# Kernel tuning notes

Measured on AMD Instinct MI355X. Metric: run time of the kernel, lower is better.

## Reference

```python
import jax, jax.numpy as jnp
import numpy as np

D = 1024   # dims
H = 16     # heads
HD = D // H  # head_dim = 64
F = HD // 2  # rotary frequency count


def _layernorm(x, g, b, eps=1e-5):
    m = x.mean(-1, keepdims=True)
    v = jnp.mean((x - m) ** 2, axis=-1, keepdims=True)
    return (x - m) * jax.lax.rsqrt(v + eps) * g + b


def _freq_base():
    # mask=None branch of rotary._compute_freqs: mel-style frequencies
    mel_max = 2595.0 * np.log10(1.0 + 4000.0 / 200.0)
    scale = 10.0 ** (np.linspace(0.0, mel_max, F) / 2595.0) - 1.0
    return jnp.asarray(200.0 * scale / 1000.0, dtype=jnp.float32)  # [F]


def _rope_polar(xh, radius, theta):
    # xh: [b,h,c,hd]; radius: [b,c] (learned per-token magnitude); theta: [c,F]
    # complex multiply of interleaved pairs by r*exp(i*theta)
    b_, h_, c_, hd_ = xh.shape
    xp = xh.reshape(b_, h_, c_, F, 2)
    xr, xi = xp[..., 0], xp[..., 1]
    cos = jnp.cos(theta)[None, None]  # [1,1,c,F]
    sin = jnp.sin(theta)[None, None]
    r = radius[:, None, :, None]      # [b,1,c,1]
    out_r = r * (xr * cos - xi * sin)
    out_i = r * (xr * sin + xi * cos)
    return jnp.stack([out_r, out_i], axis=-1).reshape(b_, h_, c_, hd_)


def setup_inputs() -> dict:
    key = jax.random.key(0)
    ks = jax.random.split(key, 6)
    B, C = 2, 2048
    s = 0.02
    return {
        "x": jax.random.normal(ks[0], (B, C, D), jnp.float32),
        "ln_q_g": jnp.ones((D,), jnp.float32),
        "ln_q_b": jnp.zeros((D,), jnp.float32),
        "Wq": jax.random.normal(ks[1], (D, D), jnp.float32) * s,
        "bq": jnp.zeros((D,), jnp.float32),
        "ln_kv_g": jnp.ones((D,), jnp.float32),
        "ln_kv_b": jnp.zeros((D,), jnp.float32),
        "Wkv": jax.random.normal(ks[2], (D, 2 * D), jnp.float32) * s,
        "bkv": jnp.zeros((2 * D,), jnp.float32),
        "Wout": jax.random.normal(ks[3], (D, D), jnp.float32) * s,
        "bout": jnp.zeros((D,), jnp.float32),
        "lnh_g": jnp.ones((HD,), jnp.float32),
        "lnh_b": jnp.zeros((HD,), jnp.float32),
        "Wr": jax.random.normal(ks[4], (D, 1), jnp.float32) * s,
        "br": jnp.zeros((1,), jnp.float32),
    }


def reference(x, ln_q_g, ln_q_b, Wq, bq, ln_kv_g, ln_kv_b, Wkv, bkv,
              Wout, bout, lnh_g, lnh_b, Wr, br):
    B, C, _ = x.shape
    # q path: norm -> linear -> [b,h,c,d]
    q = (_layernorm(x, ln_q_g, ln_q_b) @ Wq + bq).reshape(B, C, H, HD).transpose(0, 2, 1, 3)
    # kv path: norm -> linear -> [2,b,h,c,d]
    kv = (_layernorm(x, ln_kv_g, ln_kv_b) @ Wkv + bkv).reshape(B, C, 2, H, HD).transpose(2, 0, 3, 1, 4)
    k, v = kv[0], kv[1]
    # polar RoPE with learned per-token radius (xa = x for both q and k)
    t = jnp.arange(C, dtype=jnp.float32)
    theta = t[:, None] * _freq_base()[None, :]               # [C,F]
    per_step = (x @ Wr + br)[..., 0]                         # [B,C]
    radius = jnp.clip(per_step / 100.0, 0.5, 2.0)
    q = _rope_polar(q, radius, theta)
    k = _rope_polar(k, radius, theta)
    # per-head LayerNorm fused into SDPA inputs
    qn = _layernorm(q, lnh_g, lnh_b)
    kn = _layernorm(k, lnh_g, lnh_b)
    # non-causal SDPA (torch default scale = 1/sqrt(head_dim))
    logits = jnp.einsum('bhqd,bhkd->bhqk', qn, kn) / jnp.sqrt(jnp.float32(HD))
    attn = jax.nn.softmax(logits, axis=-1)
    o = jnp.einsum('bhqk,bhkd->bhqd', attn, v)
    o = o.transpose(0, 2, 1, 3).reshape(B, C, D)
    return o @ Wout + bout
```

## Files before the change

kernel.cpp:

```cpp
#include <hip/hip_runtime.h>
#include <math.h>

#define D_MODEL 1024
#define NHEADS  16
#define HEADD   64
#define NFREQ   32
#define BATCH   2
#define CSEQ    2048
#define NROWS   (BATCH*CSEQ)
#define NQKV    (3*D_MODEL)

typedef _Float16 half8  __attribute__((ext_vector_type(8)));
typedef _Float16 half4v __attribute__((ext_vector_type(4)));
typedef float    f32x4  __attribute__((ext_vector_type(4)));

__device__ __forceinline__ void async16(void* lds, const void* g)
{
    __builtin_amdgcn_global_load_lds((const __attribute__((address_space(1))) unsigned int*)g,
                                     (__attribute__((address_space(3))) unsigned int*)lds,
                                     16, 0, 0);
}

__global__ __launch_bounds__(256) void build_cs_kernel(float2* __restrict__ cs)
{
    int i = blockIdx.x * 256 + threadIdx.x;
    if (i >= CSEQ * NFREQ) return;
    int c = i >> 5, f = i & (NFREQ - 1);
    double mel_max = 2595.0 * log10(21.0);
    double step    = mel_max / (double)(NFREQ - 1);
    double freq    = 200.0 * (pow(10.0, step * (double)f / 2595.0) - 1.0) / 1000.0;
    float fr = (float)freq;
    float th = (float)c * fr;
    float s, co;
    sincosf(th, &s, &co);
    cs[i] = make_float2(co, s);
}

__global__ __launch_bounds__(256) void bias_init_kernel(
    const float* __restrict__ bq, const float* __restrict__ bkv, float* __restrict__ be)
{
    int i = blockIdx.x * 256 + threadIdx.x;
    if (i < D_MODEL) be[i] = bq[i];
    else if (i < NQKV) be[i] = bkv[i - D_MODEL];
}

__global__ __launch_bounds__(256) void transpose_fold_kernel(
    const float* __restrict__ in, _Float16* __restrict__ out, int R, int C,
    int rowoff, const float* __restrict__ scale,
    const float* __restrict__ bfold, float* __restrict__ bias_acc)
{
    __shared__ float t[32][33];
    __shared__ float part[4][32];
    int bx = blockIdx.x * 32;
    int by = blockIdx.y * 32;
    int tx = threadIdx.x, ty = threadIdx.y;
    #pragma unroll
    for (int i = ty; i < 32; i += 8)
        t[i][tx] = in[(size_t)(by + i) * C + bx + tx];
    __syncthreads();
    float sc = scale ? scale[by + tx] : 1.f;
    #pragma unroll
    for (int i = ty; i < 32; i += 8)
        out[(size_t)(rowoff + bx + i) * R + by + tx] = (_Float16)(t[tx][i] * sc);
    if (bfold) {
        float p = 0.f;
        #pragma unroll
        for (int i = ty; i < 32; i += 8)
            p += bfold[by + i] * t[i][tx];
        p += __shfl_xor(p, 32);
        if ((ty & 1) == 0) part[ty >> 1][tx] = p;
        __syncthreads();
        if (ty == 0)
            atomicAdd(&bias_acc[rowoff + bx + tx],
                      part[0][tx] + part[1][tx] + part[2][tx] + part[3][tx]);
    }
}

__global__ __launch_bounds__(256) void ln_radius_kernel(
    const float* __restrict__ x,
    const float* __restrict__ Wr,  const float* __restrict__ br,
    _Float16* __restrict__ xn, float* __restrict__ radius)
{
    int row = blockIdx.x;
    int tid = threadIdx.x;
    float4 xv = ((const float4*)(x + (size_t)row * D_MODEL))[tid];
    float4 wv = ((const float4*)Wr)[tid];
    float s  = xv.x + xv.y + xv.z + xv.w;
    float ss = xv.x*xv.x + xv.y*xv.y + xv.z*xv.z + xv.w*xv.w;
    float dr = xv.x*wv.x + xv.y*wv.y + xv.z*wv.z + xv.w*wv.w;
    #pragma unroll
    for (int off = 1; off < 64; off <<= 1) {
        s  += __shfl_xor(s, off);
        ss += __shfl_xor(ss, off);
        dr += __shfl_xor(dr, off);
    }
    __shared__ float red[3][4];
    int w = tid >> 6, lane = tid & 63;
    if (lane == 0) { red[0][w] = s; red[1][w] = ss; red[2][w] = dr; }
    __syncthreads();
    s  = red[0][0] + red[0][1] + red[0][2] + red[0][3];
    ss = red[1][0] + red[1][1] + red[1][2] + red[1][3];
    float mean = s * (1.f / D_MODEL);
    float var  = ss * (1.f / D_MODEL) - mean * mean;
    float rinv = rsqrtf(var + 1e-5f);
    half4v o4 = { (_Float16)((xv.x - mean) * rinv), (_Float16)((xv.y - mean) * rinv),
                  (_Float16)((xv.z - mean) * rinv), (_Float16)((xv.w - mean) * rinv) };
    *(half4v*)&xn[(size_t)row * D_MODEL + tid * 4] = o4;
    if (tid == 0) {
        float drt = red[2][0] + red[2][1] + red[2][2] + red[2][3];
        float p = (drt + br[0]) * 0.01f;
        radius[row] = fminf(fmaxf(p, 0.5f), 2.0f);
    }
}

__device__ __forceinline__ void gemm_core32(
    const _Float16* __restrict__ A, const _Float16* __restrict__ B,
    int bm, int bn, int K, _Float16* As, _Float16* Bs, f32x4 (*acc)[4])
{
    int tid = threadIdx.x, lane = tid & 63, w = tid >> 6;
    int wm = w >> 1, wn = w & 1;
    int l15 = lane & 15, lg = lane >> 4;
    int sr  = lane >> 2;
    int sch = lane & 3;

    auto stage = [&](int buf, int k0) {
        #pragma unroll
        for (int i = 0; i < 2; ++i) {
            int seg = w * 2 + i;
            int row = seg * 16 + sr;
            async16(&As[buf * 4096 + seg * 512], &A[(size_t)(bm + row) * K + k0 + sch * 8]);
            async16(&Bs[buf * 4096 + seg * 512], &B[(size_t)(bn + row) * K + k0 + sch * 8]);
        }
    };

    stage(0, 0);
    __syncthreads();
    int cur = 0;
    for (int k0 = 0; k0 < K; k0 += 32) {
        if (k0 + 32 < K) stage(cur ^ 1, k0 + 32);
        half8 af[4], bf[4];
        #pragma unroll
        for (int m = 0; m < 4; ++m)
            af[m] = *(const half8*)&As[cur * 4096 + (wm * 64 + m * 16 + l15) * 32 + lg * 8];
        #pragma unroll
        for (int n = 0; n < 4; ++n)
            bf[n] = *(const half8*)&Bs[cur * 4096 + (wn * 64 + n * 16 + l15) * 32 + lg * 8];
        #pragma unroll
        for (int m = 0; m < 4; ++m)
            #pragma unroll
            for (int n = 0; n < 4; ++n)
                acc[m][n] = __builtin_amdgcn_mfma_f32_16x16x32_f16(af[m], bf[n], acc[m][n], 0, 0, 0);
        __syncthreads();
        cur ^= 1;
    }
}

#define QSCALE 0.18033688f

__global__ __launch_bounds__(256, 4) void gemm_qkv_kernel(
    const _Float16* __restrict__ xn,  const _Float16* __restrict__ WT,
    const float* __restrict__ bias_eff,
    const float* __restrict__ radius, const float2* __restrict__ cs_tab,
    const float* __restrict__ lnh_g,  const float* __restrict__ lnh_b,
    _Float16* __restrict__ qn, _Float16* __restrict__ kn, _Float16* __restrict__ v_rm)
{
    __shared__ _Float16 As[2 * 4096];
    __shared__ _Float16 Bs[2 * 4096];
    int orig = blockIdx.x;
    int wg = (orig & 7) * 96 + (orig >> 3);
    int bm = (wg / 24) * 128;
    int bn = (wg % 24) * 128;

    f32x4 acc[4][4];
    f32x4 z = {0.f, 0.f, 0.f, 0.f};
    #pragma unroll
    for (int m = 0; m < 4; ++m)
        #pragma unroll
        for (int n = 0; n < 4; ++n) acc[m][n] = z;

    gemm_core32(xn, WT, bm, bn, D_MODEL, As, Bs, acc);

    int tid = threadIdx.x, lane = tid & 63, w = tid >> 6;
    int wm = w >> 1, wn = w & 1;
    int l15 = lane & 15, lg = lane >> 4;
    int colbase = bn + wn * 64;

    float bb4[4];
    #pragma unroll
    for (int n = 0; n < 4; ++n) bb4[n] = bias_eff[colbase + n * 16 + l15];

    if (colbase >= 2 * D_MODEL) {
        int vcolb = colbase - 2 * D_MODEL;
        #pragma unroll
        for (int m = 0; m < 4; ++m)
            #pragma unroll
            for (int r = 0; r < 4; ++r) {
                int row = bm + wm * 64 + m * 16 + lg * 4 + r;
                #pragma unroll
                for (int n = 0; n < 4; ++n)
                    v_rm[(size_t)row * D_MODEL + vcolb + n * 16 + l15] =
                        (_Float16)(acc[m][n][r] + bb4[n]);
            }
        return;
    }

    bool isq = colbase < D_MODEL;
    int h = (colbase & (D_MODEL - 1)) >> 6;
    _Float16* dst = isq ? qn : kn;
    float qs = isq ? QSCALE : 1.f;
    bool im = (l15 & 1) != 0;

    float g4[4], bh4[4];
    #pragma unroll
    for (int n = 0; n < 4; ++n) {
        g4[n]  = lnh_g[n * 16 + l15];
        bh4[n] = lnh_b[n * 16 + l15];
    }

    #pragma unroll
    for (int m = 0; m < 4; ++m)
        #pragma unroll
        for (int r = 0; r < 4; ++r) {
            int row = bm + wm * 64 + m * 16 + lg * 4 + r;
            int b = row >> 11, c = row & (CSEQ - 1);
            float rr = radius[row];
            float vals[4];
            float s = 0.f, ss = 0.f;
            #pragma unroll
            for (int n = 0; n < 4; ++n) {
                float v0 = acc[m][n][r] + bb4[n];
                float pr = __shfl_xor(v0, 1);
                float2 cs = cs_tab[c * NFREQ + ((n * 16 + l15) >> 1)];
                float xr_ = im ? pr : v0;
                float xi_ = im ? v0 : pr;
                float rot = im ? rr * (xr_ * cs.y + xi_ * cs.x)
                               : rr * (xr_ * cs.x - xi_ * cs.y);
                vals[n] = rot;
                s += rot; ss += rot * rot;
            }
            #pragma unroll
            for (int off = 1; off < 16; off <<= 1) {
                s  += __shfl_xor(s, off);
                ss += __shfl_xor(ss, off);
            }
            float mean = s * (1.f / 64.f);
            float var  = ss * (1.f / 64.f) - mean * mean;
            float ri   = rsqrtf(var + 1e-5f);
            size_t base = ((size_t)(b * NHEADS + h) * CSEQ + c) * HEADD;
            #pragma unroll
            for (int n = 0; n < 4; ++n) {
                float o = ((vals[n] - mean) * ri * g4[n] + bh4[n]) * qs;
                dst[base + n * 16 + l15] = (_Float16)o;
            }
        }
}

__global__ __launch_bounds__(256, 4) void gemm_out_kernel(
    const _Float16* __restrict__ A, const _Float16* __restrict__ BT,
    const float* __restrict__ bias, float* __restrict__ C)
{
    __shared__ _Float16 As[2 * 4096];
    __shared__ _Float16 Bs[2 * 4096];
    int orig = blockIdx.x;
    int wg = (orig & 7) * 32 + (orig >> 3);
    int bm = (wg >> 3) * 128;
    int bn = (wg & 7) * 128;

    f32x4 acc[4][4];
    f32x4 z = {0.f, 0.f, 0.f, 0.f};
    #pragma unroll
    for (int m = 0; m < 4; ++m)
        #pragma unroll
        for (int n = 0; n < 4; ++n) acc[m][n] = z;

    gemm_core32(A, BT, bm, bn, D_MODEL, As, Bs, acc);

    int tid = threadIdx.x, lane = tid & 63, w = tid >> 6;
    int wm = w >> 1, wn = w & 1;
    int l15 = lane & 15, lg = lane >> 4;
    #pragma unroll
    for (int m = 0; m < 4; ++m) {
        int row = bm + wm * 64 + m * 16 + lg * 4;
        #pragma unroll
        for (int n = 0; n < 4; ++n) {
            int col = bn + wn * 64 + n * 16 + l15;
            float bb = bias[col];
            #pragma unroll
            for (int r = 0; r < 4; ++r)
                C[(size_t)(row + r) * D_MODEL + col] = acc[m][n][r] + bb;
        }
    }
}

__global__ __launch_bounds__(256) void v_transpose_f16(
    const _Float16* __restrict__ v_rm, _Float16* __restrict__ vT)
{
    int bh = blockIdx.x >> 5;
    int c0 = (blockIdx.x & 31) * 64;
    int b = bh >> 4, h = bh & 15;
    __shared__ _Float16 t[64][68];
    int tid = threadIdx.x;
    int dcol = tid & 63, quarter = tid >> 6;
    for (int c = quarter; c < 64; c += 4)
        t[c][dcol] = v_rm[(size_t)(b * CSEQ + c0 + c) * D_MODEL + h * HEADD + dcol];
    __syncthreads();
    for (int d = quarter; d < 64; d += 4)
        vT[(size_t)(bh * HEADD + d) * CSEQ + c0 + dcol] = t[dcol][d];
}

#define KVB 64
#define NT  (CSEQ / KVB)
#define C8L2E 11.541560f

__global__ __launch_bounds__(256, 4) void attn_kernel(
    const _Float16* __restrict__ qn, const _Float16* __restrict__ kn,
    const _Float16* __restrict__ vT, _Float16* __restrict__ o)
{
    __shared__ _Float16 KsB[2][KVB * 64];
    __shared__ _Float16 VsB[2][KVB * 64];
    __shared__ _Float16 P[4][16 * 64];
    int tid = threadIdx.x, lane = tid & 63, w = tid >> 6;
    int l15 = lane & 15, lg = lane >> 4;

    int orig = blockIdx.x;
    int wg   = (orig & 7) * 128 + (orig >> 3);
    int bh   = wg >> 5;
    int qc   = wg & 31;
    int q0   = qc * 64 + w * 16;

    const _Float16* qh = qn + (size_t)bh * CSEQ * HEADD;
    const _Float16* kh = kn + (size_t)bh * CSEQ * HEADD;
    const _Float16* vh = vT + (size_t)bh * HEADD * CSEQ;

    half8 aq[2];
    #pragma unroll
    for (int ks = 0; ks < 2; ++ks)
        aq[ks] = *(const half8*)&qh[(size_t)(q0 + l15) * HEADD + ks * 32 + lg * 8];

    f32x4 z = {0.f, 0.f, 0.f, 0.f};
    f32x4 oacc[4];
    #pragma unroll
    for (int d4 = 0; d4 < 4; ++d4) oacc[d4] = z;
    float lrun = 0.f;

    int srow_in = lane >> 3;
    int csrc    = (lane & 7) ^ srow_in;
    int lsw     = l15 & 7;

    auto stage = [&](int buf, int kt) {
        int k0 = kt * KVB;
        #pragma unroll
        for (int i = 0; i < 2; ++i) {
            int seg = w * 2 + i;
            int r = seg * 8 + srow_in;
            async16(&KsB[buf][seg * 512], &kh[(size_t)(k0 + r) * HEADD + csrc * 8]);
            async16(&VsB[buf][seg * 512], &vh[(size_t)r * CSEQ + k0 + csrc * 8]);
        }
    };

    stage(0, 0);
    __syncthreads();
    int cur = 0;

    for (int kt = 0; kt < NT; ++kt) {
        if (kt + 1 < NT) stage(cur ^ 1, kt + 1);

        f32x4 st[4];
        #pragma unroll
        for (int n = 0; n < 4; ++n) st[n] = f32x4{-C8L2E, -C8L2E, -C8L2E, -C8L2E};
        #pragma unroll
        for (int ks = 0; ks < 2; ++ks) {
            half8 ak[4];
            #pragma unroll
            for (int n = 0; n < 4; ++n) {
                int row = n * 16 + l15;
                int ch = (ks * 4 + lg) ^ (row & 7);
                ak[n] = *(const half8*)&KsB[cur][row * 64 + ch * 8];
            }
            #pragma unroll
            for (int n = 0; n < 4; ++n)
                st[n] = __builtin_amdgcn_mfma_f32_16x16x32_f16(ak[n], aq[ks], st[n], 0, 0, 0);
        }

        float ps = 0.f;
        #pragma unroll
        for (int n = 0; n < 4; ++n)
            #pragma unroll
            for (int r = 0; r < 4; ++r) {
                float e = exp2f(st[n][r]);
                st[n][r] = e;
                ps += e;
            }
        ps += __shfl_xor(ps, 16);
        ps += __shfl_xor(ps, 32);
        lrun += ps;

        #pragma unroll
        for (int n = 0; n < 4; ++n) {
            half4v pk;
            #pragma unroll
            for (int r = 0; r < 4; ++r) pk[r] = (_Float16)st[n][r];
            int t  = n * 2 + (lg >> 1);
            int tp = t ^ lsw;
            *(half4v*)&P[w][l15 * 64 + tp * 8 + (lg & 1) * 4] = pk;
        }

        #pragma unroll
        for (int ks = 0; ks < 2; ++ks) {
            int tp2 = (ks * 4 + lg) ^ lsw;
            half8 ap = *(const half8*)&P[w][l15 * 64 + tp2 * 8];
            half8 bv[4];
            #pragma unroll
            for (int d4 = 0; d4 < 4; ++d4) {
                int row = d4 * 16 + l15;
                int ch = (ks * 4 + lg) ^ (row & 7);
                bv[d4] = *(const half8*)&VsB[cur][row * 64 + ch * 8];
            }
            #pragma unroll
            for (int d4 = 0; d4 < 4; ++d4)
                oacc[d4] = __builtin_amdgcn_mfma_f32_16x16x32_f16(ap, bv[d4], oacc[d4], 0, 0, 0);
        }

        __syncthreads();
        cur ^= 1;
    }

    int b = bh >> 4, h = bh & 15;
    #pragma unroll
    for (int r = 0; r < 4; ++r) {
        float lr = __shfl(lrun, lg * 4 + r);
        float inv = 1.f / lr;
        int c = q0 + lg * 4 + r;
        size_t base = ((size_t)b * CSEQ + c) * D_MODEL + h * HEADD;
        #pragma unroll
        for (int d4 = 0; d4 < 4; ++d4)
            o[base + d4 * 16 + l15] = (_Float16)(oacc[d4][r] * inv);
    }
}

extern "C" void kernel_launch(void* const* d_in, const int* in_sizes, int n_in,
                              void* d_out, int out_size, void* d_ws, size_t ws_size,
                              hipStream_t stream)
{
    (void)in_sizes; (void)n_in; (void)out_size; (void)ws_size;
    const float* x      = (const float*)d_in[0];
    const float* ln_q_g = (const float*)d_in[1];
    const float* ln_q_b = (const float*)d_in[2];
    const float* Wq     = (const float*)d_in[3];
    const float* bq     = (const float*)d_in[4];
    const float* ln_kv_g= (const float*)d_in[5];
    const float* ln_kv_b= (const float*)d_in[6];
    const float* Wkv    = (const float*)d_in[7];
    const float* bkv    = (const float*)d_in[8];
    const float* Wout   = (const float*)d_in[9];
    const float* bout   = (const float*)d_in[10];
    const float* lnh_g  = (const float*)d_in[11];
    const float* lnh_b  = (const float*)d_in[12];
    const float* Wr     = (const float*)d_in[13];
    const float* br     = (const float*)d_in[14];
    float* out = (float*)d_out;

    char* ws = (char*)d_ws;
    size_t off = 0;
    auto alloc = [&](size_t bytes) -> void* {
        void* p = ws + off;
        off += (bytes + 255) & ~(size_t)255;
        return p;
    };
    _Float16* WqkvT  = (_Float16*)alloc((size_t)NQKV * D_MODEL * 2);
    _Float16* WoutT  = (_Float16*)alloc((size_t)D_MODEL * D_MODEL * 2);
    float*    bias_e = (float*)   alloc((size_t)NQKV * 4);
    float*    radius = (float*)   alloc((size_t)NROWS * 4);
    float2*   cs_tab = (float2*)  alloc((size_t)CSEQ * NFREQ * 8);
    _Float16* vT     = (_Float16*)alloc((size_t)BATCH * NHEADS * HEADD * CSEQ * 2);
    _Float16* v_rm   = (_Float16*)alloc((size_t)NROWS * D_MODEL * 2);
    _Float16* xn     = (_Float16*)alloc((size_t)NROWS * D_MODEL * 2);
    _Float16* qn     = (_Float16*)alloc((size_t)NROWS * D_MODEL * 2);
    _Float16* kn     = (_Float16*)alloc((size_t)NROWS * D_MODEL * 2);
    _Float16* o_h    = (_Float16*)alloc((size_t)NROWS * D_MODEL * 2);

    hipLaunchKernelGGL(bias_init_kernel, dim3(NQKV / 256), dim3(256), 0, stream, bq, bkv, bias_e);
    hipLaunchKernelGGL(build_cs_kernel, dim3(CSEQ * NFREQ / 256), dim3(256), 0, stream, cs_tab);
    hipLaunchKernelGGL(transpose_fold_kernel, dim3(D_MODEL/32, D_MODEL/32), dim3(32, 8), 0, stream,
                       Wq, WqkvT, D_MODEL, D_MODEL, 0, ln_q_g, ln_q_b, bias_e);
    hipLaunchKernelGGL(transpose_fold_kernel, dim3(2*D_MODEL/32, D_MODEL/32), dim3(32, 8), 0, stream,
                       Wkv, WqkvT, D_MODEL, 2*D_MODEL, D_MODEL, ln_kv_g, ln_kv_b, bias_e);
    hipLaunchKernelGGL(transpose_fold_kernel, dim3(D_MODEL/32, D_MODEL/32), dim3(32, 8), 0, stream,
                       Wout, WoutT, D_MODEL, D_MODEL, 0, (const float*)nullptr,
                       (const float*)nullptr, (float*)nullptr);
    hipLaunchKernelGGL(ln_radius_kernel, dim3(NROWS), dim3(256), 0, stream,
                       x, Wr, br, xn, radius);
    hipLaunchKernelGGL(gemm_qkv_kernel, dim3(768), dim3(256), 0, stream,
                       xn, WqkvT, bias_e, radius, cs_tab, lnh_g, lnh_b, qn, kn, v_rm);
    hipLaunchKernelGGL(v_transpose_f16, dim3(BATCH*NHEADS*CSEQ/64), dim3(256), 0, stream,
                       v_rm, vT);
    hipLaunchKernelGGL(attn_kernel, dim3(BATCH*NHEADS*CSEQ/64), dim3(256), 0, stream,
                       qn, kn, vT, o_h);
    hipLaunchKernelGGL(gemm_out_kernel, dim3(256), dim3(256), 0, stream,
                       o_h, WoutT, bout, out);
}
```

Before: 160.4 us.

## Double query rows per wave and keep softmax probabilities in registers for PV

Each wave now processes 32 query rows instead of 16, so every K and V fragment read from shared memory feeds twice as many MFMAs, and the grid is halved. The P tile no longer round-trips through shared memory: the exp'd scores are packed straight into register operands for a 16x16x16 MFMA with V as the A operand, which removes the LDS write and read for P. Row-sum reductions move out of the loop to the epilogue, and the output is written as half4 vectors. In exchange register pressure rises (launch bounds drop to 2 blocks per SIMD group), there are fewer workgroups, and the PV step uses a narrower-K MFMA.

```diff
diff --git a/kernel.cpp b/kernel.cpp
--- a/kernel.cpp
+++ b/kernel.cpp
@@ -312,40 +312,43 @@
 #define NT  (CSEQ / KVB)
 #define C8L2E 11.541560f
 
-__global__ __launch_bounds__(256, 4) void attn_kernel(
+__global__ __launch_bounds__(256, 2) void attn_kernel(
     const _Float16* __restrict__ qn, const _Float16* __restrict__ kn,
     const _Float16* __restrict__ vT, _Float16* __restrict__ o)
 {
     __shared__ _Float16 KsB[2][KVB * 64];
     __shared__ _Float16 VsB[2][KVB * 64];
-    __shared__ _Float16 P[4][16 * 64];
     int tid = threadIdx.x, lane = tid & 63, w = tid >> 6;
     int l15 = lane & 15, lg = lane >> 4;
 
     int orig = blockIdx.x;
-    int wg   = (orig & 7) * 128 + (orig >> 3);
-    int bh   = wg >> 5;
-    int qc   = wg & 31;
-    int q0   = qc * 64 + w * 16;
+    int wg   = (orig & 7) * 64 + (orig >> 3);
+    int bh   = wg >> 4;
+    int qc   = wg & 15;
+    int q0   = qc * 128 + w * 32;
 
     const _Float16* qh = qn + (size_t)bh * CSEQ * HEADD;
     const _Float16* kh = kn + (size_t)bh * CSEQ * HEADD;
     const _Float16* vh = vT + (size_t)bh * HEADD * CSEQ;
 
-    half8 aq[2];
-    #pragma unroll
-    for (int ks = 0; ks < 2; ++ks)
-        aq[ks] = *(const half8*)&qh[(size_t)(q0 + l15) * HEADD + ks * 32 + lg * 8];
+    half8 aq[2][2];
+    #pragma unroll
+    for (int m = 0; m < 2; ++m)
+        #pragma unroll
+        for (int ks = 0; ks < 2; ++ks)
+            aq[m][ks] = *(const half8*)&qh[(size_t)(q0 + m * 16 + l15) * HEADD + ks * 32 + lg * 8];
 
     f32x4 z = {0.f, 0.f, 0.f, 0.f};
-    f32x4 oacc[4];
-    #pragma unroll
-    for (int d4 = 0; d4 < 4; ++d4) oacc[d4] = z;
-    float lrun = 0.f;
+    f32x4 oacc[2][4];
+    #pragma unroll
+    for (int m = 0; m < 2; ++m)
+        #pragma unroll
+        for (int db = 0; db < 4; ++db) oacc[m][db] = z;
+    float lrun[2] = {0.f, 0.f};
 
     int srow_in = lane >> 3;
     int csrc    = (lane & 7) ^ srow_in;
-    int lsw     = l15 & 7;
+    int l7      = l15 & 7;
 
     auto stage = [&](int buf, int kt) {
         int k0 = kt * KVB;
@@ -365,60 +368,50 @@
     for (int kt = 0; kt < NT; ++kt) {
         if (kt + 1 < NT) stage(cur ^ 1, kt + 1);
 
-        f32x4 st[4];
-        #pragma unroll
-        for (int n = 0; n < 4; ++n) st[n] = f32x4{-C8L2E, -C8L2E, -C8L2E, -C8L2E};
+        f32x4 st[2][4];
+        #pragma unroll
+        for (int m = 0; m < 2; ++m)
+            #pragma unroll
+            for (int n = 0; n < 4; ++n) st[m][n] = f32x4{-C8L2E, -C8L2E, -C8L2E, -C8L2E};
         #pragma unroll
         for (int ks = 0; ks < 2; ++ks) {
             half8 ak[4];
             #pragma unroll
+            for (int n = 0; n < 4; ++n)
+                ak[n] = *(const half8*)&KsB[cur][(n * 16 + l15) * 64 + ((ks * 4 + lg) ^ l7) * 8];
+            #pragma unroll
+            for (int m = 0; m < 2; ++m)
+                #pragma unroll
+                for (int n = 0; n < 4; ++n)
+                    st[m][n] = __builtin_amdgcn_mfma_f32_16x16x32_f16(ak[n], aq[m][ks], st[m][n], 0, 0, 0);
+        }
+
+        half4v bp[2][4];
+        #pragma unroll
+        for (int m = 0; m < 2; ++m)
+            #pragma unroll
             for (int n = 0; n < 4; ++n) {
-                int row = n * 16 + l15;
-                int ch = (ks * 4 + lg) ^ (row & 7);
-                ak[n] = *(const half8*)&KsB[cur][row * 64 + ch * 8];
-            }
-            #pragma unroll
-            for (int n = 0; n < 4; ++n)
-                st[n] = __builtin_amdgcn_mfma_f32_16x16x32_f16(ak[n], aq[ks], st[n], 0, 0, 0);
-        }
-
-        float ps = 0.f;
-        #pragma unroll
-        for (int n = 0; n < 4; ++n)
-            #pragma unroll
-            for (int r = 0; r < 4; ++r) {
-                float e = exp2f(st[n][r]);
-                st[n][r] = e;
-                ps += e;
-            }
-        ps += __shfl_xor(ps, 16);
-        ps += __shfl_xor(ps, 32);
-        lrun += ps;
+                float p0 = exp2f(st[m][n][0]), p1 = exp2f(st[m][n][1]);
+                float p2 = exp2f(st[m][n][2]), p3 = exp2f(st[m][n][3]);
+                lrun[m] += (p0 + p1) + (p2 + p3);
+                half4v pk = { (_Float16)p0, (_Float16)p1, (_Float16)p2, (_Float16)p3 };
+                bp[m][n] = pk;
+            }
 
         #pragma unroll
         for (int n = 0; n < 4; ++n) {
-            half4v pk;
-            #pragma unroll
-            for (int r = 0; r < 4; ++r) pk[r] = (_Float16)st[n][r];
-            int t  = n * 2 + (lg >> 1);
-            int tp = t ^ lsw;
-            *(half4v*)&P[w][l15 * 64 + tp * 8 + (lg & 1) * 4] = pk;
-        }
-
-        #pragma unroll
-        for (int ks = 0; ks < 2; ++ks) {
-            int tp2 = (ks * 4 + lg) ^ lsw;
-            half8 ap = *(const half8*)&P[w][l15 * 64 + tp2 * 8];
-            half8 bv[4];
-            #pragma unroll
-            for (int d4 = 0; d4 < 4; ++d4) {
-                int row = d4 * 16 + l15;
-                int ch = (ks * 4 + lg) ^ (row & 7);
-                bv[d4] = *(const half8*)&VsB[cur][row * 64 + ch * 8];
-            }
-            #pragma unroll
-            for (int d4 = 0; d4 < 4; ++d4)
-                oacc[d4] = __builtin_amdgcn_mfma_f32_16x16x32_f16(ap, bv[d4], oacc[d4], 0, 0, 0);
+            half4v av[4];
+            #pragma unroll
+            for (int db = 0; db < 4; ++db) {
+                int row = db * 16 + l15;
+                int ch = (2 * n + (lg >> 1)) ^ l7;
+                av[db] = *(const half4v*)&VsB[cur][row * 64 + ch * 8 + (lg & 1) * 4];
+            }
+            #pragma unroll
+            for (int m = 0; m < 2; ++m)
+                #pragma unroll
+                for (int db = 0; db < 4; ++db)
+                    oacc[m][db] = __builtin_amdgcn_mfma_f32_16x16x16f16(av[db], bp[m][n], oacc[m][db], 0, 0, 0);
         }
 
         __syncthreads();
@@ -427,14 +420,19 @@
 
     int b = bh >> 4, h = bh & 15;
     #pragma unroll
-    for (int r = 0; r < 4; ++r) {
-        float lr = __shfl(lrun, lg * 4 + r);
-        float inv = 1.f / lr;
-        int c = q0 + lg * 4 + r;
+    for (int m = 0; m < 2; ++m) {
+        float l = lrun[m];
+        l += __shfl_xor(l, 16);
+        l += __shfl_xor(l, 32);
+        float inv = 1.f / l;
+        int c = q0 + m * 16 + l15;
         size_t base = ((size_t)b * CSEQ + c) * D_MODEL + h * HEADD;
         #pragma unroll
-        for (int d4 = 0; d4 < 4; ++d4)
-            o[base + d4 * 16 + l15] = (_Float16)(oacc[d4][r] * inv);
+        for (int db = 0; db < 4; ++db) {
+            half4v ov = { (_Float16)(oacc[m][db][0] * inv), (_Float16)(oacc[m][db][1] * inv),
+                          (_Float16)(oacc[m][db][2] * inv), (_Float16)(oacc[m][db][3] * inv) };
+            *(half4v*)&o[base + db * 16 + lg * 4] = ov;
+        }
     }
 }
 
@@ -494,7 +492,7 @@
                        xn, WqkvT, bias_e, radius, cs_tab, lnh_g, lnh_b, qn, kn, v_rm);
     hipLaunchKernelGGL(v_transpose_f16, dim3(BATCH*NHEADS*CSEQ/64), dim3(256), 0, stream,
                        v_rm, vT);
-    hipLaunchKernelGGL(attn_kernel, dim3(BATCH*NHEADS*CSEQ/64), dim3(256), 0, stream,
+    hipLaunchKernelGGL(attn_kernel, dim3(BATCH*NHEADS*CSEQ/128), dim3(256), 0, stream,
                        qn, kn, vT, o_h);
     hipLaunchKernelGGL(gemm_out_kernel, dim3(256), dim3(256), 0, stream,
                        o_h, WoutT, bout, out);
```

After: 161.0 us. No clear change (+0.3%).
